# Kernel optimization log

Measured on AMD Instinct MI355X. Metric: run time of the kernel, lower is better.

The kernel has to match this reference:

```python
import jax, jax.numpy as jnp
import numpy as np

B, S, H = 2, 2048, 2048
NH, G = 16, 4
HD = H // NH  # 128


def setup_inputs() -> dict:
    key = jax.random.key(0)
    ks = jax.random.split(key, 9)
    sc = 0.02
    x = jax.random.normal(ks[0], (B, S, H), dtype=jnp.float32)
    # causal mask: 1.0 where j > i (masked), added as mask * -1e9 (matches torch code)
    causal_mask = jnp.triu(jnp.ones((S, S), dtype=jnp.float32), k=1)[None, None]
    Wq = jax.random.normal(ks[1], (H, H), dtype=jnp.float32) * sc
    bq = jnp.zeros((H,), dtype=jnp.float32)
    Wk = jax.random.normal(ks[2], (H, G * HD), dtype=jnp.float32) * sc
    bk = jnp.zeros((G * HD,), dtype=jnp.float32)
    Wv = jax.random.normal(ks[3], (H, G * HD), dtype=jnp.float32) * sc
    bv = jnp.zeros((G * HD,), dtype=jnp.float32)
    Wo = jax.random.normal(ks[4], (H, H), dtype=jnp.float32) * sc
    bo = jnp.zeros((H,), dtype=jnp.float32)
    return {"hidden_state": x, "causal_mask": causal_mask,
            "Wq": Wq, "bq": bq, "Wk": Wk, "bk": bk,
            "Wv": Wv, "bv": bv, "Wo": Wo, "bo": bo}


def reference(hidden_state, causal_mask, Wq, bq, Wk, bk, Wv, bv, Wo, bo):
    bsz, seq_len, _ = hidden_state.shape
    npg = NH // G  # query heads per KV group
    q = hidden_state @ Wq + bq                      # [B,S,H]
    k = hidden_state @ Wk + bk                      # [B,S,G*HD]
    v = hidden_state @ Wv + bv                      # [B,S,G*HD]
    # split heads; group query heads by KV group instead of repeating K/V
    q = q.reshape(bsz, seq_len, G, npg, HD).transpose(0, 2, 3, 1, 4)   # [B,G,npg,S,HD]
    k = k.reshape(bsz, seq_len, G, HD).transpose(0, 2, 1, 3)           # [B,G,S,HD]
    v = v.reshape(bsz, seq_len, G, HD).transpose(0, 2, 1, 3)           # [B,G,S,HD]
    scale = 1.0 / jnp.sqrt(jnp.float32(HD))
    scores = jnp.einsum('bgnsd,bgtd->bgnst', q, k) * scale             # [B,G,npg,S,S]
    scores = scores + causal_mask[:, :, None] * (-1e9)
    probs = jax.nn.softmax(scores, axis=-1)
    out = jnp.einsum('bgnst,bgtd->bgnsd', probs, v)                    # [B,G,npg,S,HD]
    out = out.transpose(0, 3, 1, 2, 4).reshape(bsz, seq_len, H)        # [B,S,H]
    return out @ Wo + bo
```

## Files before the change

### kernel.cpp

```cpp
#include <hip/hip_runtime.h>
#include <hip/hip_bf16.h>

#define B_   2
#define S_   2048
#define H_   2048
#define NH_  16
#define G_   4
#define HD_  128
#define NPG_ 4
#define MROWS_ (B_ * S_)
#define KVC_   (G_ * HD_)
#define NT_    (S_ / 64)
#define QSCALE_ 0.08838834764831845f

typedef __attribute__((ext_vector_type(8))) short bf16x8;
typedef __attribute__((ext_vector_type(4))) float f32x4;

__device__ __forceinline__ short f2bf_s(float f) {
    __hip_bfloat16 h = __float2bfloat16(f);
    short s; __builtin_memcpy(&s, &h, 2); return s;
}

__device__ __forceinline__ void gll16(const void* g, void* l) {
    __builtin_amdgcn_global_load_lds(
        (const __attribute__((address_space(1))) unsigned int*)g,
        (__attribute__((address_space(3))) unsigned int*)l, 16, 0, 0);
}

struct alignas(16) bf8pack { short s[8]; };
struct alignas(8)  s4pack  { short s[4]; };

__device__ __forceinline__ bf16x8 ld2x64(const short* p) {
    s4pack lo = *(const s4pack*)p;
    s4pack hi = *(const s4pack*)(p + 4);
    bf16x8 v;
    __builtin_memcpy(&v, &lo, 8);
    __builtin_memcpy((char*)&v + 8, &hi, 8);
    return v;
}

__device__ __forceinline__ void tile_transpose64(
    const float* __restrict__ in, __hip_bfloat16* __restrict__ out,
    int R, int C, int bx, int by, int tid) {
    __shared__ short tile[64][68];
    const int r = tid >> 2, c0 = (tid & 3) * 16;
    const float4* src = (const float4*)(in + (size_t)(by * 64 + r) * C + bx * 64 + c0);
    float4 f0 = src[0], f1 = src[1], f2 = src[2], f3 = src[3];
    short* tp = &tile[r][c0];
    tp[0]  = f2bf_s(f0.x); tp[1]  = f2bf_s(f0.y);
    tp[2]  = f2bf_s(f0.z); tp[3]  = f2bf_s(f0.w);
    tp[4]  = f2bf_s(f1.x); tp[5]  = f2bf_s(f1.y);
    tp[6]  = f2bf_s(f1.z); tp[7]  = f2bf_s(f1.w);
    tp[8]  = f2bf_s(f2.x); tp[9]  = f2bf_s(f2.y);
    tp[10] = f2bf_s(f2.z); tp[11] = f2bf_s(f2.w);
    tp[12] = f2bf_s(f3.x); tp[13] = f2bf_s(f3.y);
    tp[14] = f2bf_s(f3.z); tp[15] = f2bf_s(f3.w);
    __syncthreads();
    const int a = tid & 15, qq = tid >> 4;
    const int i0 = a * 4, j0 = qq * 4;
    s4pack r0v = *(const s4pack*)&tile[i0 + 0][j0];
    s4pack r1v = *(const s4pack*)&tile[i0 + 1][j0];
    s4pack r2v = *(const s4pack*)&tile[i0 + 2][j0];
    s4pack r3v = *(const s4pack*)&tile[i0 + 3][j0];
    #pragma unroll
    for (int c = 0; c < 4; ++c) {
        s4pack o;
        o.s[0] = r0v.s[c]; o.s[1] = r1v.s[c];
        o.s[2] = r2v.s[c]; o.s[3] = r3v.s[c];
        *(s4pack*)(out + (size_t)(bx * 64 + j0 + c) * R + by * 64 + i0) = o;
    }
}

__global__ __launch_bounds__(256) void prep(
    const float* __restrict__ x,  bf8pack* __restrict__ xb,
    const float* __restrict__ Wq, __hip_bfloat16* __restrict__ WqT,
    const float* __restrict__ Wk, __hip_bfloat16* __restrict__ WkT,
    const float* __restrict__ Wv, __hip_bfloat16* __restrict__ WvT,
    const float* __restrict__ Wo, __hip_bfloat16* __restrict__ WoT,
    const float* __restrict__ bq, const float* __restrict__ bk,
    const float* __restrict__ bv, float* __restrict__ bqkv) {
    const int bid = blockIdx.x, tid = threadIdx.x;
    if (bid < 4096) {
        int i = bid * 256 + tid;
        const float4* p = (const float4*)(x + (size_t)i * 8);
        float4 a = p[0], c = p[1];
        bf8pack o;
        o.s[0] = f2bf_s(a.x); o.s[1] = f2bf_s(a.y);
        o.s[2] = f2bf_s(a.z); o.s[3] = f2bf_s(a.w);
        o.s[4] = f2bf_s(c.x); o.s[5] = f2bf_s(c.y);
        o.s[6] = f2bf_s(c.z); o.s[7] = f2bf_s(c.w);
        xb[i] = o;
    } else if (bid < 5120) {
        int t = bid - 4096;
        tile_transpose64(Wq, WqT, H_, H_, t & 31, t >> 5, tid);
    } else if (bid < 5376) {
        int t = bid - 5120;
        tile_transpose64(Wk, WkT, H_, KVC_, t & 7, t >> 3, tid);
    } else if (bid < 5632) {
        int t = bid - 5376;
        tile_transpose64(Wv, WvT, H_, KVC_, t & 7, t >> 3, tid);
    } else if (bid < 6656) {
        int t = bid - 5632;
        tile_transpose64(Wo, WoT, H_, H_, t & 31, t >> 5, tid);
    } else {
        int i = (bid - 6656) * 256 + tid;
        if (i < 3072)
            bqkv[i] = (i < 2048) ? bq[i] : (i < 2560) ? bk[i - 2048] : bv[i - 2560];
    }
}

template <int BM, int NF>
__device__ __forceinline__ void gemm_core(
    const __hip_bfloat16* __restrict__ A,
    const __hip_bfloat16* __restrict__ Bt,
    const int K, const int bm, const int bn,
    short* __restrict__ As, short* __restrict__ Bs,
    f32x4 (* __restrict__ acc)[NF])
{
    constexpr int MH  = BM / 64;
    constexpr int AI  = BM / 64;
    constexpr int NB2 = NF - 2;
    constexpr int STG = AI + NF;
    constexpr int ASZ = BM * 64;
    constexpr int BSZ = 64 * NF * 64;
    const int t0 = threadIdx.x;
    const int lane = t0 & 63, wave = t0 >> 6;
    const int l15 = lane & 15, quad = lane >> 4;
    const int lrow = lane >> 3, lcg = lane & 7;
    const int wm = (wave >> 2) * (BM / 2);
    const int wn = (wave & 3) * (16 * NF);
    const int nt = K >> 6;

    auto stage = [&](int ti) {
        const int kt = ti << 6;
        short* Ad = As + (ti & 1) * ASZ;
        short* Bd = Bs + (ti & 1) * BSZ;
        #pragma unroll
        for (int p = 0; p < AI; ++p) {
            const int r0 = wave * (AI * 8) + p * 8;
            const int row = r0 + lrow;
            gll16(A + (size_t)(bm + row) * K + kt + ((lcg ^ (row & 7)) << 3),
                  Ad + r0 * 64);
        }
        #pragma unroll
        for (int p = 0; p < NF; ++p) {
            const int r0 = wave * (NF * 8) + p * 8;
            const int row = r0 + lrow;
            gll16(Bt + (size_t)(bn + row) * K + kt + ((lcg ^ (row & 7)) << 3),
                  Bd + r0 * 64);
        }
    };

    auto waitcnt_stg = [&]() {
        if constexpr (STG == 7)      asm volatile("s_waitcnt vmcnt(7)" ::: "memory");
        else if constexpr (STG == 6) asm volatile("s_waitcnt vmcnt(6)" ::: "memory");
        else if constexpr (STG == 8) asm volatile("s_waitcnt vmcnt(8)" ::: "memory");
        else                         asm volatile("s_waitcnt vmcnt(0)" ::: "memory");
    };

    stage(0); stage(1);
    waitcnt_stg();
    asm volatile("s_barrier" ::: "memory");

    for (int t = 0; t < nt; ++t) {
        const short* Ab = As + (t & 1) * ASZ;
        const short* Bb = Bs + (t & 1) * BSZ;
        bf16x8 bg1[2][2], bg2[NB2][2], ah[MH][2];

        #pragma unroll
        for (int n = 0; n < 2; ++n) {
            const int rb = wn + n * 16 + l15;
            #pragma unroll
            for (int ks = 0; ks < 2; ++ks)
                bg1[n][ks] = *(const bf16x8*)(Bb + rb * 64 +
                    (((ks * 4 + quad) ^ (rb & 7)) << 3));
        }
        #pragma unroll
        for (int i = 0; i < MH; ++i) {
            const int ra = wm + i * 16 + l15;
            #pragma unroll
            for (int ks = 0; ks < 2; ++ks)
                ah[i][ks] = *(const bf16x8*)(Ab + ra * 64 +
                    (((ks * 4 + quad) ^ (ra & 7)) << 3));
        }
        asm volatile("s_barrier" ::: "memory");
        asm volatile("s_waitcnt lgkmcnt(0)" ::: "memory");
        __builtin_amdgcn_s_setprio(1);
        #pragma unroll
        for (int ks = 0; ks < 2; ++ks)
            #pragma unroll
            for (int i = 0; i < MH; ++i)
                #pragma unroll
                for (int n = 0; n < 2; ++n)
                    acc[i][n] = __builtin_amdgcn_mfma_f32_16x16x32_bf16(
                        ah[i][ks], bg1[n][ks], acc[i][n], 0, 0, 0);
        __builtin_amdgcn_s_setprio(0);
        asm volatile("s_barrier" ::: "memory");

        #pragma unroll
        for (int n = 0; n < NB2; ++n) {
            const int rb = wn + (2 + n) * 16 + l15;
            #pragma unroll
            for (int ks = 0; ks < 2; ++ks)
                bg2[n][ks] = *(const bf16x8*)(Bb + rb * 64 +
                    (((ks * 4 + quad) ^ (rb & 7)) << 3));
        }
        asm volatile("s_barrier" ::: "memory");
        asm volatile("s_waitcnt lgkmcnt(0)" ::: "memory");
        __builtin_amdgcn_s_setprio(1);
        #pragma unroll
        for (int ks = 0; ks < 2; ++ks)
            #pragma unroll
            for (int i = 0; i < MH; ++i)
                #pragma unroll
                for (int n = 0; n < NB2; ++n)
                    acc[i][2 + n] = __builtin_amdgcn_mfma_f32_16x16x32_bf16(
                        ah[i][ks], bg2[n][ks], acc[i][2 + n], 0, 0, 0);
        __builtin_amdgcn_s_setprio(0);
        asm volatile("s_barrier" ::: "memory");

        #pragma unroll
        for (int i = 0; i < MH; ++i) {
            const int ra = wm + (MH + i) * 16 + l15;
            #pragma unroll
            for (int ks = 0; ks < 2; ++ks)
                ah[i][ks] = *(const bf16x8*)(Ab + ra * 64 +
                    (((ks * 4 + quad) ^ (ra & 7)) << 3));
        }
        asm volatile("s_barrier" ::: "memory");
        asm volatile("s_waitcnt lgkmcnt(0)" ::: "memory");
        __builtin_amdgcn_s_setprio(1);
        #pragma unroll
        for (int ks = 0; ks < 2; ++ks)
            #pragma unroll
            for (int i = 0; i < MH; ++i)
                #pragma unroll
                for (int n = 0; n < NB2; ++n)
                    acc[MH + i][2 + n] = __builtin_amdgcn_mfma_f32_16x16x32_bf16(
                        ah[i][ks], bg2[n][ks], acc[MH + i][2 + n], 0, 0, 0);
        __builtin_amdgcn_s_setprio(0);
        asm volatile("s_barrier" ::: "memory");

        if (t + 2 < nt) stage(t + 2);
        __builtin_amdgcn_s_setprio(1);
        #pragma unroll
        for (int ks = 0; ks < 2; ++ks)
            #pragma unroll
            for (int i = 0; i < MH; ++i)
                #pragma unroll
                for (int n = 0; n < 2; ++n)
                    acc[MH + i][n] = __builtin_amdgcn_mfma_f32_16x16x32_bf16(
                        ah[i][ks], bg1[n][ks], acc[MH + i][n], 0, 0, 0);
        __builtin_amdgcn_s_setprio(0);

        if (t + 2 < nt) {
            waitcnt_stg();
            asm volatile("s_barrier" ::: "memory");
        } else if (t + 1 < nt) {
            asm volatile("s_waitcnt vmcnt(0)" ::: "memory");
            asm volatile("s_barrier" ::: "memory");
        }
    }
}

__global__ __launch_bounds__(512, 2) void gemm_qkv8(
    const __hip_bfloat16* __restrict__ A,
    const __hip_bfloat16* __restrict__ Bt,
    const float* __restrict__ bias,
    __hip_bfloat16* __restrict__ Qo,
    __hip_bfloat16* __restrict__ Ko,
    __hip_bfloat16* __restrict__ VtG) {
    __shared__ __align__(16) short As[2 * 256 * 64];
    __shared__ __align__(16) short Bs[2 * 192 * 64];
    const int bid = blockIdx.x;
    const int s = (bid & 7) * 32 + (bid >> 3);
    const int bm = (s & 15) * 256, bn = (s >> 4) * 192;

    f32x4 acc[8][3] = {};
    gemm_core<256, 3>(A, Bt, H_, bm, bn, As, Bs, acc);

    const int t = threadIdx.x;
    const int lane = t & 63, wave = t >> 6;
    const int l15 = lane & 15, quad = lane >> 4;
    const int wm = (wave >> 2) * 128, wn = (wave & 3) * 48;

    #pragma unroll
    for (int i = 0; i < 8; ++i) {
        int row0 = bm + wm + i * 16 + quad * 4;
        #pragma unroll
        for (int j = 0; j < 3; ++j) {
            int c0 = bn + wn + j * 16;
            int colg = c0 + l15;
            float bv = bias[colg];
            if (c0 < 2048) {
                #pragma unroll
                for (int r = 0; r < 4; ++r)
                    Qo[(size_t)(row0 + r) * H_ + colg] =
                        __float2bfloat16((acc[i][j][r] + bv) * QSCALE_);
            } else if (c0 < 2560) {
                #pragma unroll
                for (int r = 0; r < 4; ++r)
                    Ko[(size_t)(row0 + r) * KVC_ + (colg - 2048)] =
                        __float2bfloat16(acc[i][j][r] + bv);
            } else {
                int coll = colg - 2560;
                short s4v[4];
                #pragma unroll
                for (int r = 0; r < 4; ++r) s4v[r] = f2bf_s(acc[i][j][r] + bv);
                *(uint2*)(&VtG[(size_t)coll * MROWS_ + row0]) = *(uint2*)s4v;
            }
        }
    }
}

__global__ __launch_bounds__(512, 2) void gemm_out8(
    const __hip_bfloat16* __restrict__ A,
    const __hip_bfloat16* __restrict__ Bt,
    const float* __restrict__ bias,
    float* __restrict__ C) {
    __shared__ __align__(16) short As[2 * 128 * 64];
    __shared__ __align__(16) short Bs[2 * 256 * 64];
    const int bid = blockIdx.x;
    const int s = (bid & 7) * 32 + (bid >> 3);
    const int bm = (s & 31) * 128, bn = (s >> 5) * 256;

    f32x4 acc[4][4] = {};
    gemm_core<128, 4>(A, Bt, H_, bm, bn, As, Bs, acc);

    const int t = threadIdx.x;
    const int lane = t & 63, wave = t >> 6;
    const int l15 = lane & 15, quad = lane >> 4;
    const int wm = (wave >> 2) * 64, wn = (wave & 3) * 64;

    #pragma unroll
    for (int i = 0; i < 4; ++i) {
        int row0 = bm + wm + i * 16 + quad * 4;
        #pragma unroll
        for (int j = 0; j < 4; ++j) {
            int col = bn + wn + j * 16 + l15;
            float bv = bias[col];
            #pragma unroll
            for (int r = 0; r < 4; ++r)
                C[(size_t)(row0 + r) * H_ + col] = acc[i][j][r] + bv;
        }
    }
}

__global__ __launch_bounds__(256, 2) void attn_causal_gqa(
    const __hip_bfloat16* __restrict__ Q,
    const __hip_bfloat16* __restrict__ K,
    const __hip_bfloat16* __restrict__ VtG,
    __hip_bfloat16* __restrict__ O) {
    __shared__ short KsL[2][64 * 128];
    __shared__ short VtL[128 * 64];
    __shared__ short Ps[4][2][16 * 76];

    const int h  = blockIdx.x;
    const int b  = h >> 4;
    const int hh = h & 15;
    const int g  = hh >> 2;
    const int qb1 = blockIdx.y;
    const int qb2 = NT_ - 1 - qb1;

    const int t = threadIdx.x;
    const int lane = t & 63, wave = t >> 6;
    const int l15 = lane & 15, quad = lane >> 4;
    const int swz = l15 & 7;

    const __hip_bfloat16* Qb = Q + (size_t)b * S_ * H_ + hh * HD_;
    const __hip_bfloat16* Kb = K + (size_t)b * S_ * KVC_ + g * HD_;
    const __hip_bfloat16* Vg = VtG + (size_t)g * HD_ * MROWS_ + b * S_;

    auto stageK = [&](int tile) {
        short* kd = &KsL[tile & 1][0];
        #pragma unroll
        for (int p = 0; p < 4; ++p) {
            int R0 = wave * 16 + p * 4;
            int row = R0 + (lane >> 4);
            int cg = ((lane & 15) ^ (row & 7)) * 8;
            gll16(Kb + (size_t)(tile * 64 + row) * KVC_ + cg, &kd[R0 * 128]);
        }
    };
    auto stageV = [&](int tile) {
        #pragma unroll
        for (int p = 0; p < 4; ++p) {
            int R0 = wave * 32 + p * 8;
            int row = R0 + (lane >> 3);
            int cg = ((lane & 7) ^ (row & 7)) * 8;
            gll16(Vg + (size_t)row * MROWS_ + tile * 64 + cg, &VtL[R0 * 64]);
        }
    };

    bf16x8 aq1[4], aq2[4];
    {
        const int qr1 = qb1 * 64 + wave * 16 + l15;
        const int qr2 = qb2 * 64 + wave * 16 + l15;
        #pragma unroll
        for (int kk = 0; kk < 4; ++kk) {
            aq1[kk] = *(const bf16x8*)(Qb + (size_t)qr1 * H_ + kk * 32 + quad * 8);
            aq2[kk] = *(const bf16x8*)(Qb + (size_t)qr2 * H_ + kk * 32 + quad * 8);
        }
    }

    f32x4 o1[8] = {}, o2[8] = {};
    float lp1 = 0.f, lp2 = 0.f;
    const int qrow_loc = wave * 16 + l15;

    stageK(0);

    for (int tile = 0; tile <= qb2; ++tile) {
        const bool do1 = (tile <= qb1);
        const bool last = (tile == qb2);

        stageV(tile);
        if (!last) stageK(tile + 1);

        if (!last) asm volatile("s_waitcnt vmcnt(8)" ::: "memory");
        else       asm volatile("s_waitcnt vmcnt(4)" ::: "memory");
        asm volatile("s_barrier" ::: "memory");

        const short* kb = &KsL[tile & 1][0];

        f32x4 s2[4] = {}, s1[4] = {};
        #pragma unroll
        for (int kk = 0; kk < 4; ++kk) {
            bf16x8 bk[4];
            #pragma unroll
            for (int nt = 0; nt < 4; ++nt)
                bk[nt] = *(const bf16x8*)(
                    &kb[(nt * 16 + l15) * 128 + (((kk * 4 + quad) ^ swz) * 8)]);
            #pragma unroll
            for (int nt = 0; nt < 4; ++nt)
                s2[nt] = __builtin_amdgcn_mfma_f32_16x16x32_bf16(
                    bk[nt], aq2[kk], s2[nt], 0, 0, 0);
            if (do1) {
                #pragma unroll
                for (int nt = 0; nt < 4; ++nt)
                    s1[nt] = __builtin_amdgcn_mfma_f32_16x16x32_bf16(
                        bk[nt], aq1[kk], s1[nt], 0, 0, 0);
            }
        }

        __asm__ volatile("" ::: "memory");
        short* P2 = &Ps[wave][1][0];
        {
            const bool m2 = (tile == qb2);
            #pragma unroll
            for (int nt = 0; nt < 4; ++nt) {
                s4pack pk;
                #pragma unroll
                for (int r = 0; r < 4; ++r) {
                    float p = __expf(s2[nt][r]);
                    if (m2 && (nt * 16 + quad * 4 + r > qrow_loc)) p = 0.f;
                    lp2 += p;
                    pk.s[r] = f2bf_s(p);
                }
                *(s4pack*)&P2[l15 * 76 + nt * 16 + quad * 4] = pk;
            }
        }
        short* P1 = &Ps[wave][0][0];
        if (do1) {
            const bool m1 = (tile == qb1);
            #pragma unroll
            for (int nt = 0; nt < 4; ++nt) {
                s4pack pk;
                #pragma unroll
                for (int r = 0; r < 4; ++r) {
                    float p = __expf(s1[nt][r]);
                    if (m1 && (nt * 16 + quad * 4 + r > qrow_loc)) p = 0.f;
                    lp1 += p;
                    pk.s[r] = f2bf_s(p);
                }
                *(s4pack*)&P1[l15 * 76 + nt * 16 + quad * 4] = pk;
            }
        }
        __asm__ volatile("" ::: "memory");

        if (!last) asm volatile("s_waitcnt vmcnt(4)" ::: "memory");
        else       asm volatile("s_waitcnt vmcnt(0)" ::: "memory");
        asm volatile("s_barrier" ::: "memory");

        #pragma unroll
        for (int ks = 0; ks < 2; ++ks) {
            bf16x8 ap2 = ld2x64(&P2[l15 * 76 + ks * 32 + quad * 8]);
            bf16x8 ap1;
            if (do1) ap1 = ld2x64(&P1[l15 * 76 + ks * 32 + quad * 8]);
            #pragma unroll
            for (int n2 = 0; n2 < 8; ++n2) {
                bf16x8 bv = *(const bf16x8*)(
                    &VtL[(n2 * 16 + l15) * 64 + (((ks * 4 + quad) ^ swz) * 8)]);
                o2[n2] = __builtin_amdgcn_mfma_f32_16x16x32_bf16(
                    ap2, bv, o2[n2], 0, 0, 0);
                if (do1)
                    o1[n2] = __builtin_amdgcn_mfma_f32_16x16x32_bf16(
                        ap1, bv, o1[n2], 0, 0, 0);
            }
        }
        asm volatile("s_barrier" ::: "memory");
    }

    float L1 = lp1, L2 = lp2;
    L1 += __shfl_xor(L1, 16); L2 += __shfl_xor(L2, 16);
    L1 += __shfl_xor(L1, 32); L2 += __shfl_xor(L2, 32);
    #pragma unroll
    for (int r = 0; r < 4; ++r) {
        float i1 = 1.f / __shfl(L1, quad * 4 + r);
        float i2 = 1.f / __shfl(L2, quad * 4 + r);
        int s1r = qb1 * 64 + wave * 16 + quad * 4 + r;
        int s2r = qb2 * 64 + wave * 16 + quad * 4 + r;
        #pragma unroll
        for (int n2 = 0; n2 < 8; ++n2) {
            int d = n2 * 16 + l15;
            O[((size_t)b * S_ + s1r) * H_ + hh * HD_ + d] = __float2bfloat16(o1[n2][r] * i1);
            O[((size_t)b * S_ + s2r) * H_ + hh * HD_ + d] = __float2bfloat16(o2[n2][r] * i2);
        }
    }
}

extern "C" void kernel_launch(void* const* d_in, const int* in_sizes, int n_in,
                              void* d_out, int out_size, void* d_ws, size_t ws_size,
                              hipStream_t stream) {
    const float* x  = (const float*)d_in[0];
    const float* Wq = (const float*)d_in[2];
    const float* bq = (const float*)d_in[3];
    const float* Wk = (const float*)d_in[4];
    const float* bk = (const float*)d_in[5];
    const float* Wv = (const float*)d_in[6];
    const float* bv = (const float*)d_in[7];
    const float* Wo = (const float*)d_in[8];
    const float* bo = (const float*)d_in[9];
    float* out = (float*)d_out;

    char* ws = (char*)d_ws;
    const size_t MB = 1024 * 1024;
    __hip_bfloat16* xb   = (__hip_bfloat16*)(ws);
    __hip_bfloat16* WT   = (__hip_bfloat16*)(ws + 16 * MB);
    __hip_bfloat16* Kws  = (__hip_bfloat16*)(ws + 28 * MB);
    __hip_bfloat16* VtG  = (__hip_bfloat16*)(ws + 32 * MB);
    __hip_bfloat16* WoT  = (__hip_bfloat16*)(ws + 36 * MB);
    float*          bqkv = (float*)         (ws + 44 * MB);
    __hip_bfloat16* Aws  = (__hip_bfloat16*)(ws);
    __hip_bfloat16* Qbuf = (__hip_bfloat16*)d_out;

    prep<<<6669, 256, 0, stream>>>(
        x, (bf8pack*)xb,
        Wq, WT,
        Wk, WT + (size_t)2048 * H_,
        Wv, WT + (size_t)2560 * H_,
        Wo, WoT,
        bq, bk, bv, bqkv);

    gemm_qkv8<<<256, 512, 0, stream>>>(xb, WT, bqkv, Qbuf, Kws, VtG);

    attn_causal_gqa<<<dim3(B_ * NH_, NT_ / 2), 256, 0, stream>>>(Qbuf, Kws, VtG, Aws);

    gemm_out8<<<256, 512, 0, stream>>>(Aws, WoT, bo, out);
}
```

Measured before the change: 305.5 us.

## Retile output GEMM, single-buffer attention K for higher occupancy, vectorize LDS stores

The output projection GEMM now uses a new 256x128 tile core with two N fragments per wave, processing the M rows in two halves per k-step. The attention kernel drops K double-buffering, interleaving K and V prefetch of the next tile after the current tile is consumed, and raises launch bounds to three blocks per CU. The transpose prep packs bf16 values and writes them to LDS as 8-byte stores. These aim to raise GEMM data reuse and attention occupancy, at the risk of less overlap between loads and compute in attention.

```diff
diff --git a/kernel.cpp b/kernel.cpp
--- a/kernel.cpp
+++ b/kernel.cpp
@@ -46,15 +46,20 @@
     const int r = tid >> 2, c0 = (tid & 3) * 16;
     const float4* src = (const float4*)(in + (size_t)(by * 64 + r) * C + bx * 64 + c0);
     float4 f0 = src[0], f1 = src[1], f2 = src[2], f3 = src[3];
+    short pk0[16];
+    pk0[0]  = f2bf_s(f0.x); pk0[1]  = f2bf_s(f0.y);
+    pk0[2]  = f2bf_s(f0.z); pk0[3]  = f2bf_s(f0.w);
+    pk0[4]  = f2bf_s(f1.x); pk0[5]  = f2bf_s(f1.y);
+    pk0[6]  = f2bf_s(f1.z); pk0[7]  = f2bf_s(f1.w);
+    pk0[8]  = f2bf_s(f2.x); pk0[9]  = f2bf_s(f2.y);
+    pk0[10] = f2bf_s(f2.z); pk0[11] = f2bf_s(f2.w);
+    pk0[12] = f2bf_s(f3.x); pk0[13] = f2bf_s(f3.y);
+    pk0[14] = f2bf_s(f3.z); pk0[15] = f2bf_s(f3.w);
     short* tp = &tile[r][c0];
-    tp[0]  = f2bf_s(f0.x); tp[1]  = f2bf_s(f0.y);
-    tp[2]  = f2bf_s(f0.z); tp[3]  = f2bf_s(f0.w);
-    tp[4]  = f2bf_s(f1.x); tp[5]  = f2bf_s(f1.y);
-    tp[6]  = f2bf_s(f1.z); tp[7]  = f2bf_s(f1.w);
-    tp[8]  = f2bf_s(f2.x); tp[9]  = f2bf_s(f2.y);
-    tp[10] = f2bf_s(f2.z); tp[11] = f2bf_s(f2.w);
-    tp[12] = f2bf_s(f3.x); tp[13] = f2bf_s(f3.y);
-    tp[14] = f2bf_s(f3.z); tp[15] = f2bf_s(f3.w);
+    *(s4pack*)(tp)      = *(s4pack*)(pk0);
+    *(s4pack*)(tp + 4)  = *(s4pack*)(pk0 + 4);
+    *(s4pack*)(tp + 8)  = *(s4pack*)(pk0 + 8);
+    *(s4pack*)(tp + 12) = *(s4pack*)(pk0 + 12);
     __syncthreads();
     const int a = tid & 15, qq = tid >> 4;
     const int i0 = a * 4, j0 = qq * 4;
@@ -263,6 +268,113 @@
     }
 }
 
+__device__ __forceinline__ void gemm_core_nf2(
+    const __hip_bfloat16* __restrict__ A,
+    const __hip_bfloat16* __restrict__ Bt,
+    const int K, const int bm, const int bn,
+    short* __restrict__ As, short* __restrict__ Bs,
+    f32x4 (* __restrict__ acc)[2])
+{
+    constexpr int ASZ = 256 * 64;
+    constexpr int BSZ = 128 * 64;
+    const int t0 = threadIdx.x;
+    const int lane = t0 & 63, wave = t0 >> 6;
+    const int l15 = lane & 15, quad = lane >> 4;
+    const int lrow = lane >> 3, lcg = lane & 7;
+    const int wm = (wave >> 2) * 128;
+    const int wn = (wave & 3) * 32;
+    const int nt = K >> 6;
+
+    auto stage = [&](int ti) {
+        const int kt = ti << 6;
+        short* Ad = As + (ti & 1) * ASZ;
+        short* Bd = Bs + (ti & 1) * BSZ;
+        #pragma unroll
+        for (int p = 0; p < 4; ++p) {
+            const int r0 = wave * 32 + p * 8;
+            const int row = r0 + lrow;
+            gll16(A + (size_t)(bm + row) * K + kt + ((lcg ^ (row & 7)) << 3),
+                  Ad + r0 * 64);
+        }
+        #pragma unroll
+        for (int p = 0; p < 2; ++p) {
+            const int r0 = wave * 16 + p * 8;
+            const int row = r0 + lrow;
+            gll16(Bt + (size_t)(bn + row) * K + kt + ((lcg ^ (row & 7)) << 3),
+                  Bd + r0 * 64);
+        }
+    };
+
+    stage(0); stage(1);
+    asm volatile("s_waitcnt vmcnt(6)" ::: "memory");
+    asm volatile("s_barrier" ::: "memory");
+
+    for (int t = 0; t < nt; ++t) {
+        const short* Ab = As + (t & 1) * ASZ;
+        const short* Bb = Bs + (t & 1) * BSZ;
+        bf16x8 bg[2][2], ah[4][2];
+
+        #pragma unroll
+        for (int n = 0; n < 2; ++n) {
+            const int rb = wn + n * 16 + l15;
+            #pragma unroll
+            for (int ks = 0; ks < 2; ++ks)
+                bg[n][ks] = *(const bf16x8*)(Bb + rb * 64 +
+                    (((ks * 4 + quad) ^ (rb & 7)) << 3));
+        }
+        #pragma unroll
+        for (int i = 0; i < 4; ++i) {
+            const int ra = wm + i * 16 + l15;
+            #pragma unroll
+            for (int ks = 0; ks < 2; ++ks)
+                ah[i][ks] = *(const bf16x8*)(Ab + ra * 64 +
+                    (((ks * 4 + quad) ^ (ra & 7)) << 3));
+        }
+        asm volatile("s_barrier" ::: "memory");
+        asm volatile("s_waitcnt lgkmcnt(0)" ::: "memory");
+        __builtin_amdgcn_s_setprio(1);
+        #pragma unroll
+        for (int ks = 0; ks < 2; ++ks)
+            #pragma unroll
+            for (int i = 0; i < 4; ++i)
+                #pragma unroll
+                for (int n = 0; n < 2; ++n)
+                    acc[i][n] = __builtin_amdgcn_mfma_f32_16x16x32_bf16(
+                        ah[i][ks], bg[n][ks], acc[i][n], 0, 0, 0);
+        __builtin_amdgcn_s_setprio(0);
+        asm volatile("s_barrier" ::: "memory");
+
+        #pragma unroll
+        for (int i = 0; i < 4; ++i) {
+            const int ra = wm + (4 + i) * 16 + l15;
+            #pragma unroll
+            for (int ks = 0; ks < 2; ++ks)
+                ah[i][ks] = *(const bf16x8*)(Ab + ra * 64 +
+                    (((ks * 4 + quad) ^ (ra & 7)) << 3));
+        }
+        asm volatile("s_waitcnt lgkmcnt(0)" ::: "memory");
+        asm volatile("s_barrier" ::: "memory");
+        if (t + 2 < nt) stage(t + 2);
+        __builtin_amdgcn_s_setprio(1);
+        #pragma unroll
+        for (int ks = 0; ks < 2; ++ks)
+            #pragma unroll
+            for (int i = 0; i < 4; ++i)
+                #pragma unroll
+                for (int n = 0; n < 2; ++n)
+                    acc[4 + i][n] = __builtin_amdgcn_mfma_f32_16x16x32_bf16(
+                        ah[i][ks], bg[n][ks], acc[4 + i][n], 0, 0, 0);
+        __builtin_amdgcn_s_setprio(0);
+        if (t + 2 < nt) {
+            asm volatile("s_waitcnt vmcnt(6)" ::: "memory");
+            asm volatile("s_barrier" ::: "memory");
+        } else if (t + 1 < nt) {
+            asm volatile("s_waitcnt vmcnt(0)" ::: "memory");
+            asm volatile("s_barrier" ::: "memory");
+        }
+    }
+}
+
 __global__ __launch_bounds__(512, 2) void gemm_qkv8(
     const __hip_bfloat16* __restrict__ A,
     const __hip_bfloat16* __restrict__ Bt,
@@ -318,25 +430,25 @@
     const __hip_bfloat16* __restrict__ Bt,
     const float* __restrict__ bias,
     float* __restrict__ C) {
-    __shared__ __align__(16) short As[2 * 128 * 64];
-    __shared__ __align__(16) short Bs[2 * 256 * 64];
+    __shared__ __align__(16) short As[2 * 256 * 64];
+    __shared__ __align__(16) short Bs[2 * 128 * 64];
     const int bid = blockIdx.x;
     const int s = (bid & 7) * 32 + (bid >> 3);
-    const int bm = (s & 31) * 128, bn = (s >> 5) * 256;
-
-    f32x4 acc[4][4] = {};
-    gemm_core<128, 4>(A, Bt, H_, bm, bn, As, Bs, acc);
+    const int bm = (s & 15) * 256, bn = (s >> 4) * 128;
+
+    f32x4 acc[8][2] = {};
+    gemm_core_nf2(A, Bt, H_, bm, bn, As, Bs, acc);
 
     const int t = threadIdx.x;
     const int lane = t & 63, wave = t >> 6;
     const int l15 = lane & 15, quad = lane >> 4;
-    const int wm = (wave >> 2) * 64, wn = (wave & 3) * 64;
+    const int wm = (wave >> 2) * 128, wn = (wave & 3) * 32;
 
     #pragma unroll
-    for (int i = 0; i < 4; ++i) {
+    for (int i = 0; i < 8; ++i) {
         int row0 = bm + wm + i * 16 + quad * 4;
         #pragma unroll
-        for (int j = 0; j < 4; ++j) {
+        for (int j = 0; j < 2; ++j) {
             int col = bn + wn + j * 16 + l15;
             float bv = bias[col];
             #pragma unroll
@@ -346,12 +458,12 @@
     }
 }
 
-__global__ __launch_bounds__(256, 2) void attn_causal_gqa(
+__global__ __launch_bounds__(256, 3) void attn_causal_gqa(
     const __hip_bfloat16* __restrict__ Q,
     const __hip_bfloat16* __restrict__ K,
     const __hip_bfloat16* __restrict__ VtG,
     __hip_bfloat16* __restrict__ O) {
-    __shared__ short KsL[2][64 * 128];
+    __shared__ short KsL[64 * 128];
     __shared__ short VtL[128 * 64];
     __shared__ short Ps[4][2][16 * 76];
 
@@ -372,13 +484,12 @@
     const __hip_bfloat16* Vg = VtG + (size_t)g * HD_ * MROWS_ + b * S_;
 
     auto stageK = [&](int tile) {
-        short* kd = &KsL[tile & 1][0];
         #pragma unroll
         for (int p = 0; p < 4; ++p) {
             int R0 = wave * 16 + p * 4;
             int row = R0 + (lane >> 4);
             int cg = ((lane & 15) ^ (row & 7)) * 8;
-            gll16(Kb + (size_t)(tile * 64 + row) * KVC_ + cg, &kd[R0 * 128]);
+            gll16(Kb + (size_t)(tile * 64 + row) * KVC_ + cg, &KsL[R0 * 128]);
         }
     };
     auto stageV = [&](int tile) {
@@ -406,20 +517,14 @@
     float lp1 = 0.f, lp2 = 0.f;
     const int qrow_loc = wave * 16 + l15;
 
-    stageK(0);
+    stageK(0); stageV(0);
 
     for (int tile = 0; tile <= qb2; ++tile) {
         const bool do1 = (tile <= qb1);
         const bool last = (tile == qb2);
 
-        stageV(tile);
-        if (!last) stageK(tile + 1);
-
-        if (!last) asm volatile("s_waitcnt vmcnt(8)" ::: "memory");
-        else       asm volatile("s_waitcnt vmcnt(4)" ::: "memory");
-        asm volatile("s_barrier" ::: "memory");
-
-        const short* kb = &KsL[tile & 1][0];
+        asm volatile("s_waitcnt vmcnt(4)" ::: "memory");
+        asm volatile("s_barrier" ::: "memory");
 
         f32x4 s2[4] = {}, s1[4] = {};
         #pragma unroll
@@ -428,7 +533,7 @@
             #pragma unroll
             for (int nt = 0; nt < 4; ++nt)
                 bk[nt] = *(const bf16x8*)(
-                    &kb[(nt * 16 + l15) * 128 + (((kk * 4 + quad) ^ swz) * 8)]);
+                    &KsL[(nt * 16 + l15) * 128 + (((kk * 4 + quad) ^ swz) * 8)]);
             #pragma unroll
             for (int nt = 0; nt < 4; ++nt)
                 s2[nt] = __builtin_amdgcn_mfma_f32_16x16x32_bf16(
@@ -440,6 +545,8 @@
                         bk[nt], aq1[kk], s1[nt], 0, 0, 0);
             }
         }
+        asm volatile("s_barrier" ::: "memory");
+        if (!last) stageK(tile + 1);
 
         __asm__ volatile("" ::: "memory");
         short* P2 = &Ps[wave][1][0];
@@ -497,6 +604,7 @@
             }
         }
         asm volatile("s_barrier" ::: "memory");
+        if (!last) stageV(tile + 1);
     }
 
     float L1 = lp1, L2 = lp2;
```

Measured after the change: 372.3 us. +21.9%, slower.
